# Kernel tuning notes

Hardware: AMD Instinct MI355X
Metric: run time of the kernel (lower is better)

Reference implementation:

```python
import jax, jax.numpy as jnp
import numpy as np

N = 50000      # nodes
E = 800000     # edges
IN = 32        # raw node feature dim
PE = 15        # laplacian PE dim (k)
HID = 128      # hidden
HEADS = 4
C = HID // HEADS
G = 64         # graphs in batch
L = 4          # num layers (shared weights!)


def setup_inputs() -> dict:
    key = jax.random.key(0)
    ks = jax.random.split(key, 24)
    s = 0.05
    p = lambda k, shape: jax.random.normal(k, shape, dtype=jnp.float32) * s
    inp = {
        "x": jax.random.normal(ks[0], (N, IN), dtype=jnp.float32),
        "edge_index": jax.random.randint(ks[1], (2, E), 0, N, dtype=jnp.int32),
        "batch": jnp.sort(jax.random.randint(ks[2], (N,), 0, G, dtype=jnp.int32)),
        "lap_pe": jax.random.normal(ks[3], (N, PE), dtype=jnp.float32),
        # node_in: Linear(IN+PE -> HID)
        "node_in_w": p(ks[4], (HID, IN + PE)), "node_in_b": p(ks[5], (HID,)),
        # shared TransformerConv params
        "Wq": p(ks[6], (HID, HID)), "bq": p(ks[7], (HID,)),
        "Wk": p(ks[8], (HID, HID)), "bk": p(ks[9], (HID,)),
        "Wv": p(ks[10], (HID, HID)), "bv": p(ks[11], (HID,)),
        "Wskip": p(ks[12], (HID, HID)), "bskip": p(ks[13], (HID,)),
        "Wbeta": p(ks[14], (1, 3 * HID)),  # bias=False in PyG
        # attentional aggregation gate: Linear(HID,HID)->ReLU->Linear(HID,1)
        "g1_w": p(ks[15], (HID, HID)), "g1_b": p(ks[16], (HID,)),
        "g2_w": p(ks[17], (1, HID)), "g2_b": p(ks[18], (1,)),
        # readout: Linear(HID,HID)->ReLU->Linear(HID,1)
        "r1_w": p(ks[19], (HID, HID)), "r1_b": p(ks[20], (HID,)),
        "r2_w": p(ks[21], (1, HID)), "r2_b": p(ks[22], (1,)),
    }
    return inp


def _transformer_conv(x, src, dst, Wq, bq, Wk, bk, Wv, bv, Wskip, bskip, Wbeta):
    # projections -> [N, HEADS, C]
    q = (x @ Wq.T + bq).reshape(N, HEADS, C)
    k = (x @ Wk.T + bk).reshape(N, HEADS, C)
    v = (x @ Wv.T + bv).reshape(N, HEADS, C)
    # edge attention logits: [E, HEADS]
    alpha = jnp.einsum('ehc,ehc->eh', q[dst], k[src]) / jnp.sqrt(jnp.float32(C))
    # segment softmax over destination node
    amax = jax.ops.segment_max(alpha, dst, num_segments=N)        # [N, HEADS]
    ex = jnp.exp(alpha - amax[dst])
    denom = jax.ops.segment_sum(ex, dst, num_segments=N)          # [N, HEADS]
    attn = ex / denom[dst]                                        # [E, HEADS]
    # weighted scatter-add of values
    msg = v[src] * attn[:, :, None]                               # [E, HEADS, C]
    out = jax.ops.segment_sum(msg, dst, num_segments=N).reshape(N, HID)
    # beta-gated skip connection (beta=True, root_weight=True)
    x_r = x @ Wskip.T + bskip
    beta = jax.nn.sigmoid(jnp.concatenate([out, x_r, out - x_r], axis=-1) @ Wbeta.T)
    return beta * x_r + (1.0 - beta) * out


def reference(x, edge_index, batch, lap_pe, node_in_w, node_in_b,
              Wq, bq, Wk, bk, Wv, bv, Wskip, bskip, Wbeta,
              g1_w, g1_b, g2_w, g2_b, r1_w, r1_b, r2_w, r2_b):
    src, dst = edge_index[0], edge_index[1]
    h = jnp.concatenate([x, lap_pe], axis=-1) @ node_in_w.T + node_in_b  # [N, HID]
    for _ in range(L):  # same conv instance reused -> shared weights
        h = jax.nn.relu(h + _transformer_conv(h, src, dst, Wq, bq, Wk, bk,
                                              Wv, bv, Wskip, bskip, Wbeta))
    # attentional aggregation over graphs
    gate = jax.nn.relu(h @ g1_w.T + g1_b) @ g2_w.T + g2_b                # [N, 1]
    gmax = jax.ops.segment_max(gate, batch, num_segments=G)
    gex = jnp.exp(gate - gmax[batch])
    gden = jax.ops.segment_sum(gex, batch, num_segments=G)
    w = gex / gden[batch]                                                # [N, 1]
    g = jax.ops.segment_sum(w * h, batch, num_segments=G)                # [G, HID]
    out = jax.nn.relu(g @ r1_w.T + r1_b) @ r2_w.T + r2_b                 # [G, 1]
    return out.squeeze(-1)
```

## Files before the change

kernel.cpp:

```cpp
#include <hip/hip_runtime.h>

#define NN 50000
#define EE 800000
#define INF 32
#define PEF 15
#define HID 128
#define GG 64
#define NLAYERS 4
#define NBLK 196
#define NBUCK 49
#define ECH 4096
#define EBLK 196

typedef __bf16 bf16;
typedef __attribute__((ext_vector_type(8))) bf16 bf16x8;
typedef __attribute__((ext_vector_type(4))) float f32x4;
typedef __attribute__((ext_vector_type(2))) float f32x2;

__device__ __forceinline__ float wave_allsum(float v) {
  #pragma unroll
  for (int off = 1; off < 64; off <<= 1) v += __shfl_xor(v, off);
  return v;
}

__device__ __forceinline__ float bflo(unsigned u) {
  return __builtin_bit_cast(float, u << 16);
}
__device__ __forceinline__ float bfhi(unsigned u) {
  return __builtin_bit_cast(float, u & 0xffff0000u);
}
__device__ __forceinline__ unsigned short f2bf(float v) {
  unsigned b = __builtin_bit_cast(unsigned, v);
  unsigned r = (b + 0x7fffu + ((b >> 16) & 1u)) >> 16;
  return (unsigned short)r;
}
__device__ __forceinline__ unsigned bfpack(float lo, float hi) {
  return (unsigned)f2bf(lo) | ((unsigned)f2bf(hi) << 16);
}
__device__ __forceinline__ unsigned fp8pack4(float a, float b, float c, float d) {
  unsigned lo = (unsigned)__builtin_amdgcn_cvt_pk_fp8_f32(a, b, 0, false) & 0xffffu;
  unsigned hi = (unsigned)__builtin_amdgcn_cvt_pk_fp8_f32(c, d, 0, false) & 0xffffu;
  return lo | (hi << 16);
}

__global__ void pack_weights_kernel(const float* __restrict__ Wq, const float* __restrict__ Wk,
                                    const float* __restrict__ Wv, const float* __restrict__ Ws,
                                    const float* __restrict__ bq, const float* __restrict__ bk,
                                    const float* __restrict__ bv, const float* __restrict__ bs,
                                    unsigned short* __restrict__ Wcatb, float* __restrict__ bcat) {
  int idx = blockIdx.x * blockDim.x + threadIdx.x;
  if (idx >= 512 * 128) return;
  int o = idx >> 7, j = idx & 127;
  int w = o >> 7, r = o & 127;
  const float* W = (w == 0) ? Wq : (w == 1) ? Wk : (w == 2) ? Wv : Ws;
  Wcatb[idx] = f2bf(W[r * 128 + j]);
  if (j == 0) {
    const float* b = (w == 0) ? bq : (w == 1) ? bk : (w == 2) ? bv : bs;
    bcat[o] = b[r];
  }
}

__global__ void pack_nwtb_kernel(const float* __restrict__ niw, unsigned short* __restrict__ nwtb) {
  int idx = blockIdx.x * blockDim.x + threadIdx.x;
  if (idx >= 128 * 64) return;
  int n = idx >> 6, j = idx & 63;
  nwtb[idx] = (j < INF + PEF) ? f2bf(niw[n * (INF + PEF) + j]) : (unsigned short)0;
}

__global__ void pack_g1_kernel(const float* __restrict__ g1w, unsigned short* __restrict__ g1wb) {
  int idx = blockIdx.x * blockDim.x + threadIdx.x;
  if (idx >= 128 * 128) return;
  g1wb[idx] = f2bf(g1w[idx]);
}

__global__ __launch_bounds__(256) void xpe_pack_kernel(const float* __restrict__ x,
    const float* __restrict__ pe, unsigned* __restrict__ xpeb4) {
  int n = blockIdx.x * 256 + threadIdx.x;
  if (n >= NN) return;
  unsigned ou[32];
  const float4* xr = (const float4*)(x + (size_t)n * INF);
  #pragma unroll
  for (int i = 0; i < 8; i++) {
    float4 v = xr[i];
    ou[2 * i] = bfpack(v.x, v.y);
    ou[2 * i + 1] = bfpack(v.z, v.w);
  }
  const float* pr = pe + (size_t)n * PEF;
  float p[16];
  #pragma unroll
  for (int i = 0; i < PEF; i++) p[i] = pr[i];
  p[15] = 0.f;
  #pragma unroll
  for (int i = 0; i < 8; i++) ou[16 + i] = bfpack(p[2 * i], p[2 * i + 1]);
  #pragma unroll
  for (int i = 24; i < 32; i++) ou[i] = 0u;
  unsigned* dst = xpeb4 + (size_t)n * 32;
  #pragma unroll
  for (int i = 0; i < 8; i++) ((uint4*)dst)[i] = *(uint4*)&ou[4 * i];
}

__global__ __launch_bounds__(256) void nodein_gemm_kernel(
    const bf16* __restrict__ A, const bf16* __restrict__ B,
    const float* __restrict__ bias, int M,
    float* __restrict__ h, unsigned* __restrict__ hbf4) {
  __shared__ float lds[128 * 64];
  const int t = threadIdx.x;
  const int w = t >> 6, lane = t & 63;
  const int m0 = blockIdx.x * 128;
  const int n0 = blockIdx.y * 64;
  const int lrow = lane & 15, lk = (lane >> 4) * 8;
  int ra = m0 + w * 32 + lrow;      if (ra > M - 1) ra = M - 1;
  int rb = m0 + w * 32 + 16 + lrow; if (rb > M - 1) rb = M - 1;
  const bf16* a0p = A + (size_t)ra * 64 + lk;
  const bf16* a1p = A + (size_t)rb * 64 + lk;
  const bf16* bp  = B + (size_t)(n0 + lrow) * 64 + lk;
  f32x4 acc[2][4] = {};
  #pragma unroll
  for (int ks = 0; ks < 2; ks++) {
    bf16x8 a0 = *(const bf16x8*)(a0p + ks * 32);
    bf16x8 a1 = *(const bf16x8*)(a1p + ks * 32);
    #pragma unroll
    for (int nj = 0; nj < 4; nj++) {
      bf16x8 b = *(const bf16x8*)(bp + (size_t)nj * 1024 + ks * 32);
      acc[0][nj] = __builtin_amdgcn_mfma_f32_16x16x32_bf16(a0, b, acc[0][nj], 0, 0, 0);
      acc[1][nj] = __builtin_amdgcn_mfma_f32_16x16x32_bf16(a1, b, acc[1][nj], 0, 0, 0);
    }
  }
  const int rbase = (lane >> 4) * 4;
  #pragma unroll
  for (int mi = 0; mi < 2; mi++) {
    #pragma unroll
    for (int nj = 0; nj < 4; nj++) {
      #pragma unroll
      for (int r = 0; r < 4; r++) {
        int ml = w * 32 + mi * 16 + rbase + r;
        int col = nj * 16 + lrow;
        lds[ml * 64 + (col ^ ((ml & 7) << 2))] = acc[mi][nj][r] + bias[n0 + col];
      }
    }
  }
  __syncthreads();
  #pragma unroll
  for (int kk = 0; kk < 2; kk++) {
    int u = t + kk * 256;
    int r = u & 127, s = u >> 7;
    int m = m0 + r;
    if (m >= M) continue;
    float ff[16];
    #pragma unroll
    for (int j = 0; j < 4; j++) {
      int c = s * 16 + j * 4;
      *(float4*)(ff + j * 4) = *(const float4*)(lds + r * 64 + (c ^ ((r & 7) << 2)));
    }
    int c0 = n0 + s * 16;
    float4* hp = (float4*)(h + (size_t)m * 128 + c0);
    #pragma unroll
    for (int j = 0; j < 4; j++) hp[j] = *(float4*)(ff + j * 4);
    unsigned o[8];
    #pragma unroll
    for (int i = 0; i < 8; i++) o[i] = bfpack(ff[2 * i], ff[2 * i + 1]);
    uint4* hb = (uint4*)(hbf4 + (size_t)m * 64 + (c0 >> 1));
    hb[0] = *(uint4*)&o[0];
    hb[1] = *(uint4*)&o[4];
  }
}

__global__ void count_kernel(const int* __restrict__ dst, int* __restrict__ counts) {
  int e = blockIdx.x * blockDim.x + threadIdx.x;
  if (e >= EE) return;
  atomicAdd(&counts[dst[e]], 1);
}

__global__ __launch_bounds__(256) void bsum_kernel(const int* __restrict__ counts,
                                                   int* __restrict__ bsum) {
  int b = blockIdx.x, t = threadIdx.x;
  int i = b * 256 + t;
  int v = (i < NN) ? counts[i] : 0;
  #pragma unroll
  for (int off = 1; off < 64; off <<= 1) v += __shfl_xor(v, off);
  __shared__ int red[4];
  if ((t & 63) == 0) red[t >> 6] = v;
  __syncthreads();
  if (t == 0) bsum[b] = red[0] + red[1] + red[2] + red[3];
}

__global__ void bscan_kernel(const int* __restrict__ bsum, int* __restrict__ bbase) {
  int lane = threadIdx.x;
  int carry = 0;
  for (int c = 0; c < NBLK; c += 64) {
    int i = c + lane;
    int v = (i < NBLK) ? bsum[i] : 0;
    int x = v;
    #pragma unroll
    for (int off = 1; off < 64; off <<= 1) {
      int u = __shfl_up(x, off);
      if (lane >= off) x += u;
    }
    if (i < NBLK) bbase[i] = carry + x - v;
    carry += __shfl(x, 63);
  }
}

__global__ __launch_bounds__(256) void rowptr_kernel(const int* __restrict__ counts,
    const int* __restrict__ bbase, int* __restrict__ row_ptr) {
  int b = blockIdx.x, t = threadIdx.x;
  int lane = t & 63, wid = t >> 6;
  int i = b * 256 + t;
  int v = (i < NN) ? counts[i] : 0;
  int x = v;
  #pragma unroll
  for (int off = 1; off < 64; off <<= 1) {
    int u = __shfl_up(x, off);
    if (lane >= off) x += u;
  }
  __shared__ int wsum[4];
  if (lane == 63) wsum[wid] = x;
  __syncthreads();
  int offs = bbase[b];
  for (int k = 0; k < wid; k++) offs += wsum[k];
  int incl = offs + x;
  if (i < NN) row_ptr[i + 1] = incl;
  if (b == 0 && t == 0) row_ptr[0] = 0;
}

__global__ __launch_bounds__(256) void binhist_kernel(const int* __restrict__ dst,
                                                      int* __restrict__ blockHist) {
  __shared__ int hist[NBUCK];
  int t = threadIdx.x;
  if (t < NBUCK) hist[t] = 0;
  __syncthreads();
  int base = blockIdx.x * ECH;
  int end = base + ECH; if (end > EE) end = EE;
  for (int i = base + t; i < end; i += 256) atomicAdd(&hist[dst[i] >> 10], 1);
  __syncthreads();
  if (t < NBUCK) blockHist[blockIdx.x * NBUCK + t] = hist[t];
}

__global__ void bscan2_kernel(const int* __restrict__ blockHist,
    int* __restrict__ blockBase, int* __restrict__ bucket_base) {
  int t = threadIdx.x;
  int tot = 0;
  if (t < NBUCK)
    for (int b = 0; b < EBLK; b++) tot += blockHist[b * NBUCK + t];
  int x = tot;
  #pragma unroll
  for (int off = 1; off < 64; off <<= 1) {
    int u = __shfl_up(x, off);
    if (t >= off) x += u;
  }
  int excl = x - tot;
  if (t < NBUCK) bucket_base[t] = excl;
  if (t == NBUCK - 1) bucket_base[NBUCK] = excl + tot;
  if (t < NBUCK) {
    int run = excl;
    for (int b = 0; b < EBLK; b++) {
      blockBase[b * NBUCK + t] = run;
      run += blockHist[b * NBUCK + t];
    }
  }
}

__global__ __launch_bounds__(256) void binwrite_kernel(const int* __restrict__ src,
    const int* __restrict__ dst, const int* __restrict__ blockBase,
    unsigned* __restrict__ binned) {
  __shared__ int cur[NBUCK];
  int t = threadIdx.x;
  if (t < NBUCK) cur[t] = blockBase[blockIdx.x * NBUCK + t];
  __syncthreads();
  int base = blockIdx.x * ECH;
  int end = base + ECH; if (end > EE) end = EE;
  for (int i = base + t; i < end; i += 256) {
    int d = dst[i];
    int p = atomicAdd(&cur[d >> 10], 1);
    binned[p] = (unsigned)src[i] | ((unsigned)(d & 1023) << 16);
  }
}

__global__ __launch_bounds__(512) void scatter2_kernel(const unsigned* __restrict__ binned,
    const int* __restrict__ row_ptr, const int* __restrict__ bucket_base,
    unsigned short* __restrict__ srcs16) {
  __shared__ int cur[1024];
  int g = blockIdx.x, t = threadIdx.x;
  int nbase = g << 10;
  for (int j = t; j < 1024; j += 512) {
    int node = nbase + j;
    cur[j] = (node < NN) ? row_ptr[node] : 0;
  }
  __syncthreads();
  int s0 = bucket_base[g], s1 = bucket_base[g + 1];
  for (int i = s0 + t; i < s1; i += 512) {
    unsigned pr = binned[i];
    int p = atomicAdd(&cur[pr >> 16], 1);
    srcs16[p] = (unsigned short)(pr & 0xffffu);
  }
}

__global__ void gptr_kernel(const int* __restrict__ batch, int* __restrict__ gptr) {
  int g = threadIdx.x;
  if (g > GG) return;
  if (g == GG) { gptr[GG] = NN; return; }
  int lo = 0, hi = NN;
  while (lo < hi) {
    int mid = (lo + hi) >> 1;
    if (batch[mid] < g) lo = mid + 1; else hi = mid;
  }
  gptr[g] = lo;
}

__global__ __launch_bounds__(512) void gemm0_kernel(
    const bf16* __restrict__ A, const bf16* __restrict__ B,
    const float* __restrict__ bias, int M,
    unsigned short* __restrict__ qbb, unsigned char* __restrict__ kvb,
    unsigned short* __restrict__ xrbb) {
  __shared__ float lds[64 * 128];
  const int t = threadIdx.x;
  const int w = t >> 6, lane = t & 63;
  const int wm = w >> 2, wn = w & 3;
  const int mb = blockIdx.x * 64;
  const int m0 = mb + wm * 32;
  const int n0 = wn * 128;
  const int lrow = lane & 15, lk = (lane >> 4) * 8;
  int ra = m0 + lrow;      if (ra > M - 1) ra = M - 1;
  int rb = m0 + 16 + lrow; if (rb > M - 1) rb = M - 1;
  const bf16* a0p = A + (size_t)ra * 128 + lk;
  const bf16* a1p = A + (size_t)rb * 128 + lk;
  const bf16* bp  = B + (size_t)(n0 + lrow) * 128 + lk;
  f32x4 acc[2][8] = {};
  #pragma unroll
  for (int ks = 0; ks < 4; ks++) {
    bf16x8 a0 = *(const bf16x8*)(a0p + ks * 32);
    bf16x8 a1 = *(const bf16x8*)(a1p + ks * 32);
    #pragma unroll
    for (int nj = 0; nj < 8; nj++) {
      bf16x8 b = *(const bf16x8*)(bp + (size_t)nj * 2048 + ks * 32);
      acc[0][nj] = __builtin_amdgcn_mfma_f32_16x16x32_bf16(a0, b, acc[0][nj], 0, 0, 0);
      acc[1][nj] = __builtin_amdgcn_mfma_f32_16x16x32_bf16(a1, b, acc[1][nj], 0, 0, 0);
    }
  }
  const int rbase = (lane >> 4) * 4;
  const int rr = t & 63, ss = t >> 6;
  const int m = mb + rr;
  #pragma unroll
  for (int g = 0; g < 4; g++) {
    if (wn == g) {
      #pragma unroll
      for (int mi = 0; mi < 2; mi++) {
        #pragma unroll
        for (int nj = 0; nj < 8; nj++) {
          #pragma unroll
          for (int r = 0; r < 4; r++) {
            int row = wm * 32 + mi * 16 + rbase + r;
            int col = nj * 16 + lrow;
            lds[row * 128 + (col ^ ((row & 7) << 2))] = acc[mi][nj][r] + bias[g * 128 + col];
          }
        }
      }
    }
    __syncthreads();
    if (m < M) {
      float ff[16];
      #pragma unroll
      for (int j = 0; j < 4; j++) {
        int c = ss * 16 + j * 4;
        *(float4*)(ff + j * 4) = *(const float4*)(lds + rr * 128 + (c ^ ((rr & 7) << 2)));
      }
      int c0 = ss * 16;
      if (g == 0) {
        unsigned o[8];
        #pragma unroll
        for (int i = 0; i < 8; i++) o[i] = bfpack(ff[2 * i], ff[2 * i + 1]);
        uint4* dq = (uint4*)(qbb + (size_t)m * 128 + c0);
        dq[0] = *(uint4*)&o[0];
        dq[1] = *(uint4*)&o[4];
      } else if (g == 1 || g == 2) {
        unsigned o[4];
        #pragma unroll
        for (int i = 0; i < 4; i++)
          o[i] = fp8pack4(ff[4 * i], ff[4 * i + 1], ff[4 * i + 2], ff[4 * i + 3]);
        int cell = c0 >> 3;
        int voff = (g == 1) ? 0 : 8;
        unsigned char* bp8 = kvb + (size_t)m * 256;
        uint2 w0; w0.x = o[0]; w0.y = o[1];
        uint2 w1; w1.x = o[2]; w1.y = o[3];
        *(uint2*)(bp8 + cell * 16 + voff) = w0;
        *(uint2*)(bp8 + (cell + 1) * 16 + voff) = w1;
      } else {
        unsigned o[8];
        #pragma unroll
        for (int i = 0; i < 8; i++) o[i] = bfpack(ff[2 * i], ff[2 * i + 1]);
        uint4* dx = (uint4*)(xrbb + (size_t)m * 128 + c0);
        dx[0] = *(uint4*)&o[0];
        dx[1] = *(uint4*)&o[4];
      }
    }
    __syncthreads();
  }
}

__global__ __launch_bounds__(512) void gemm1_gate_kernel(
    const bf16* __restrict__ A, const bf16* __restrict__ B,
    const float* __restrict__ b1, const float* __restrict__ g2w,
    const float* __restrict__ g2b, int M, float* __restrict__ gx) {
  const int w = threadIdx.x >> 6, lane = threadIdx.x & 63;
  const int m0 = blockIdx.x * 128 + w * 16;
  const int lrow = lane & 15, lk = (lane >> 4) * 8;
  int ra = m0 + lrow; if (ra > M - 1) ra = M - 1;
  const bf16* ap = A + (size_t)ra * 128 + lk;
  const bf16* bp = B + (size_t)lrow * 128 + lk;
  f32x4 acc[8] = {};
  #pragma unroll
  for (int ks = 0; ks < 4; ks++) {
    bf16x8 a = *(const bf16x8*)(ap + ks * 32);
    #pragma unroll
    for (int nj = 0; nj < 8; nj++) {
      bf16x8 b = *(const bf16x8*)(bp + (size_t)nj * 2048 + ks * 32);
      acc[nj] = __builtin_amdgcn_mfma_f32_16x16x32_bf16(a, b, acc[nj], 0, 0, 0);
    }
  }
  float g2v[8], b1v[8];
  #pragma unroll
  for (int nj = 0; nj < 8; nj++) {
    g2v[nj] = g2w[nj * 16 + lrow];
    b1v[nj] = b1[nj * 16 + lrow];
  }
  const float b2 = g2b[0];
  const int rbase = (lane >> 4) * 4;
  #pragma unroll
  for (int r = 0; r < 4; r++) {
    int m = m0 + rbase + r;
    float d = 0.f;
    #pragma unroll
    for (int nj = 0; nj < 8; nj++)
      d += fmaxf(acc[nj][r] + b1v[nj], 0.f) * g2v[nj];
    d += __shfl_xor(d, 1);
    d += __shfl_xor(d, 2);
    d += __shfl_xor(d, 4);
    d += __shfl_xor(d, 8);
    if (lrow == 0 && m < M) gx[m] = __expf(d + b2);
  }
}

__global__ __launch_bounds__(256) void attn_beta_kernel(
    const unsigned short* __restrict__ qbb,
    const unsigned char* __restrict__ kvb,
    const int* __restrict__ row_ptr, const unsigned short* __restrict__ srcs,
    const unsigned* __restrict__ xrb4,
    const float* __restrict__ Wbeta,
    float* __restrict__ h, unsigned* __restrict__ hbf4) {
  __shared__ float xlds[4][128];
  const int wid = threadIdx.x >> 6;
  const int wv = blockIdx.x * 4 + wid;
  const int lane = threadIdx.x & 63;
  const int sl = lane & 15;
  const int eg = lane >> 4;
  float qf[8];
  {
    bf16x8 qv = *(const bf16x8*)((const bf16*)qbb + (size_t)wv * 128 + sl * 8);
    #pragma unroll
    for (int j = 0; j < 8; j++) qf[j] = (float)qv[j];
  }
  const int e0 = row_ptr[wv], e1 = row_ptr[wv + 1];
  const float C = 0.25503486f;
  float dex = 0.f;
  float acc[8] = {0, 0, 0, 0, 0, 0, 0, 0};

#define PROC(cell, valid)                                                   \
  {                                                                         \
    f32x2 k0 = __builtin_amdgcn_cvt_pk_f32_fp8((cell).x, false);            \
    f32x2 k1 = __builtin_amdgcn_cvt_pk_f32_fp8((cell).x, true);             \
    f32x2 k2 = __builtin_amdgcn_cvt_pk_f32_fp8((cell).y, false);            \
    f32x2 k3 = __builtin_amdgcn_cvt_pk_f32_fp8((cell).y, true);             \
    float p = qf[0] * k0.x + qf[1] * k0.y + qf[2] * k1.x + qf[3] * k1.y     \
            + qf[4] * k2.x + qf[5] * k2.y + qf[6] * k3.x + qf[7] * k3.y;    \
    p += __shfl_xor(p, 1);                                                  \
    p += __shfl_xor(p, 2);                                                  \
    float ex = (valid) ? exp2f(p * C) : 0.f;                                \
    dex += ex;                                                              \
    f32x2 v0 = __builtin_amdgcn_cvt_pk_f32_fp8((cell).z, false);            \
    f32x2 v1 = __builtin_amdgcn_cvt_pk_f32_fp8((cell).z, true);             \
    f32x2 v2 = __builtin_amdgcn_cvt_pk_f32_fp8((cell).w, false);            \
    f32x2 v3 = __builtin_amdgcn_cvt_pk_f32_fp8((cell).w, true);             \
    acc[0] += ex * v0.x; acc[1] += ex * v0.y;                               \
    acc[2] += ex * v1.x; acc[3] += ex * v1.y;                               \
    acc[4] += ex * v2.x; acc[5] += ex * v2.y;                               \
    acc[6] += ex * v3.x; acc[7] += ex * v3.y;                               \
  }

  for (int base = e0; base < e1; base += 64) {
    int rem = e1 - base;
    int cnt = rem < 64 ? rem : 64;
    int mysrc = (lane < rem) ? (int)srcs[base + lane] : 0;
    int i = 0;
    for (; i + 4 < cnt; i += 8) {
      int sea = __shfl(mysrc, i + eg);
      int seb = __shfl(mysrc, i + 4 + eg);
      uint4 ca = *(const uint4*)(kvb + (size_t)sea * 256 + sl * 16);
      uint4 cb = *(const uint4*)(kvb + (size_t)seb * 256 + sl * 16);
      PROC(ca, true);
      PROC(cb, (i + 4 + eg < cnt));
    }
    if (i < cnt) {
      int sea = __shfl(mysrc, i + eg);
      uint4 ca = *(const uint4*)(kvb + (size_t)sea * 256 + sl * 16);
      PROC(ca, (i + eg < cnt));
    }
  }
#undef PROC

  dex += __shfl_xor(dex, 16);
  dex += __shfl_xor(dex, 32);
  #pragma unroll
  for (int j = 0; j < 8; j++) {
    acc[j] += __shfl_xor(acc[j], 16);
    acc[j] += __shfl_xor(acc[j], 32);
  }
  float inv = (e1 > e0) ? 1.f / dex : 0.f;
  if (eg == 0) {
    #pragma unroll
    for (int j = 0; j < 8; j++) xlds[wid][sl * 8 + j] = acc[j] * inv;
  }
  __syncthreads();
  float ox = xlds[wid][2 * lane];
  float oy = xlds[wid][2 * lane + 1];
  unsigned xu = xrb4[(size_t)wv * 64 + lane];
  float xx = bflo(xu), xy = bfhi(xu);
  const float2* wb = (const float2*)Wbeta;
  float2 wo = wb[lane], wx = wb[64 + lane], wd = wb[128 + lane];
  float part = ox * wo.x + oy * wo.y + xx * wx.x + xy * wx.y
             + (ox - xx) * wd.x + (oy - xy) * wd.y;
  part = wave_allsum(part);
  float beta = 1.f / (1.f + __expf(-part));
  float2* hp = (float2*)(h + (size_t)wv * 128);
  float2 h2 = hp[lane];
  float r0 = fmaxf(h2.x + beta * xx + (1.f - beta) * ox, 0.f);
  float r1 = fmaxf(h2.y + beta * xy + (1.f - beta) * oy, 0.f);
  h2.x = r0; h2.y = r1;
  hp[lane] = h2;
  hbf4[(size_t)wv * 64 + lane] = bfpack(r0, r1);
}

__global__ __launch_bounds__(256) void gden_kernel(const float* __restrict__ gx,
    const int* __restrict__ gptr, float* __restrict__ gden) {
  int g = blockIdx.x, t = threadIdx.x;
  int n0 = gptr[g], n1 = gptr[g + 1];
  float s = 0.f;
  for (int n = n0 + t; n < n1; n += 256) s += gx[n];
  s = wave_allsum(s);
  __shared__ float red[4];
  if ((t & 63) == 0) red[t >> 6] = s;
  __syncthreads();
  if (t == 0) gden[g] = red[0] + red[1] + red[2] + red[3];
}

__global__ __launch_bounds__(128) void gagg_kernel(const float* __restrict__ gx,
    const float* __restrict__ h, const int* __restrict__ gptr,
    float* __restrict__ gfeat_raw) {
  int g = blockIdx.x;
  int c = blockIdx.y;
  int d = threadIdx.x;
  int n0 = gptr[g], n1 = gptr[g + 1];
  float acc = 0.f;
  for (int n = n0 + c; n < n1; n += 32) acc += gx[n] * h[(size_t)n * 128 + d];
  atomicAdd(&gfeat_raw[g * 128 + d], acc);
}

__global__ __launch_bounds__(128) void readout_kernel(const float* __restrict__ gfeat_raw,
    const float* __restrict__ gden,
    const float* __restrict__ r1w, const float* __restrict__ r1b,
    const float* __restrict__ r2w, const float* __restrict__ r2b,
    float* __restrict__ out) {
  int g = blockIdx.x;
  int u = threadIdx.x;
  __shared__ float sh[128];
  __shared__ float red[128];
  float dv = gden[g];
  float inv = (dv > 0.f) ? 1.f / dv : 0.f;
  sh[u] = gfeat_raw[g * 128 + u] * inv;
  __syncthreads();
  float tacc = r1b[u];
  for (int j = 0; j < 128; j++) tacc += sh[j] * r1w[u * 128 + j];
  tacc = fmaxf(tacc, 0.f);
  red[u] = tacc * r2w[u];
  __syncthreads();
  for (int off = 64; off > 0; off >>= 1) {
    if (u < off) red[u] += red[u + off];
    __syncthreads();
  }
  if (u == 0) out[g] = red[0] + r2b[0];
}

extern "C" void kernel_launch(void* const* d_in, const int* in_sizes, int n_in,
                              void* d_out, int out_size, void* d_ws, size_t ws_size,
                              hipStream_t stream) {
  (void)in_sizes; (void)n_in; (void)out_size; (void)ws_size;
  const float* x     = (const float*)d_in[0];
  const int*   ei    = (const int*)d_in[1];
  const int*   batch = (const int*)d_in[2];
  const float* pe    = (const float*)d_in[3];
  const float* niw   = (const float*)d_in[4];
  const float* nib   = (const float*)d_in[5];
  const float* Wq    = (const float*)d_in[6];
  const float* bq    = (const float*)d_in[7];
  const float* Wk    = (const float*)d_in[8];
  const float* bk    = (const float*)d_in[9];
  const float* Wv    = (const float*)d_in[10];
  const float* bv    = (const float*)d_in[11];
  const float* Wsk   = (const float*)d_in[12];
  const float* bsk   = (const float*)d_in[13];
  const float* Wbeta = (const float*)d_in[14];
  const float* g1w   = (const float*)d_in[15];
  const float* g1b   = (const float*)d_in[16];
  const float* g2w   = (const float*)d_in[17];
  const float* g2b   = (const float*)d_in[18];
  const float* r1w   = (const float*)d_in[19];
  const float* r1b   = (const float*)d_in[20];
  const float* r2w   = (const float*)d_in[21];
  const float* r2b   = (const float*)d_in[22];
  float* out = (float*)d_out;

  float* ws = (float*)d_ws;
  float* h     = ws; ws += (size_t)NN * 128;
  float* qbbf  = ws; ws += (size_t)NN * 64;
  float* kvbf  = ws; ws += (size_t)NN * 64;
  float* xrbf  = ws; ws += (size_t)NN * 64;
  float* hbff  = ws; ws += (size_t)NN * 64;
  float* xpebf = ws; ws += (size_t)NN * 32;
  float* Wcatf = ws; ws += 512 * 64;
  float* g1wbf = ws; ws += 128 * 64;
  float* nwtbf = ws; ws += 128 * 32;
  float* bcat  = ws; ws += 512;
  float* gx    = ws; ws += NN;
  float* gfeat = ws; ws += GG * 128;
  float* gden  = ws; ws += GG;
  int* row_ptr = (int*)ws;
  int* counts   = row_ptr + (NN + 1);
  int* bsum     = counts + NN;
  int* bbase    = bsum + NBLK;
  int* gptr     = bbase + NBLK;
  int* blockHist= gptr + (GG + 1);
  int* blockBase= blockHist + EBLK * NBUCK;
  int* bucketB  = blockBase + EBLK * NBUCK;
  unsigned* binned = (unsigned*)(bucketB + (NBUCK + 1));
  unsigned short* srcs16 = (unsigned short*)(binned + EE);

  unsigned short* qbb   = (unsigned short*)qbbf;
  unsigned char*  kvb   = (unsigned char*)kvbf;
  unsigned short* xrbb  = (unsigned short*)xrbf;
  unsigned short* hbf   = (unsigned short*)hbff;
  unsigned short* Wcatb = (unsigned short*)Wcatf;
  unsigned short* g1wb  = (unsigned short*)g1wbf;
  unsigned short* nwtb  = (unsigned short*)nwtbf;
  const int* src = ei;
  const int* dst = ei + EE;

  hipMemsetAsync(counts, 0, NN * sizeof(int), stream);
  hipMemsetAsync(gfeat, 0, GG * 128 * sizeof(float), stream);
  pack_weights_kernel<<<(512 * 128 + 255) / 256, 256, 0, stream>>>(
      Wq, Wk, Wv, Wsk, bq, bk, bv, bsk, Wcatb, bcat);
  pack_nwtb_kernel<<<(128 * 64 + 255) / 256, 256, 0, stream>>>(niw, nwtb);
  pack_g1_kernel<<<(128 * 128 + 255) / 256, 256, 0, stream>>>(g1w, g1wb);
  xpe_pack_kernel<<<NBLK, 256, 0, stream>>>(x, pe, (unsigned*)xpebf);
  count_kernel<<<(EE + 255) / 256, 256, 0, stream>>>(dst, counts);
  bsum_kernel<<<NBLK, 256, 0, stream>>>(counts, bsum);
  bscan_kernel<<<1, 64, 0, stream>>>(bsum, bbase);
  rowptr_kernel<<<NBLK, 256, 0, stream>>>(counts, bbase, row_ptr);
  binhist_kernel<<<EBLK, 256, 0, stream>>>(dst, blockHist);
  bscan2_kernel<<<1, 64, 0, stream>>>(blockHist, blockBase, bucketB);
  binwrite_kernel<<<EBLK, 256, 0, stream>>>(src, dst, blockBase, binned);
  scatter2_kernel<<<NBUCK, 512, 0, stream>>>(binned, row_ptr, bucketB, srcs16);
  gptr_kernel<<<1, 128, 0, stream>>>(batch, gptr);

  const int MB0 = (NN + 127) / 128;
  const int MB64 = (NN + 63) / 64;
  nodein_gemm_kernel<<<dim3(MB0, 2), 256, 0, stream>>>(
      (const bf16*)xpebf, (const bf16*)nwtb, nib, NN, h, (unsigned*)hbf);

  for (int l = 0; l < NLAYERS; l++) {
    gemm0_kernel<<<MB64, 512, 0, stream>>>(
        (const bf16*)hbf, (const bf16*)Wcatb, bcat, NN, qbb, kvb, xrbb);
    attn_beta_kernel<<<12500, 256, 0, stream>>>(
        qbb, kvb, row_ptr, srcs16, (const unsigned*)xrbb, Wbeta, h, (unsigned*)hbf);
  }

  gemm1_gate_kernel<<<MB0, 512, 0, stream>>>(
      (const bf16*)hbf, (const bf16*)g1wb, g1b, g2w, g2b, NN, gx);
  gden_kernel<<<GG, 256, 0, stream>>>(gx, gptr, gden);
  gagg_kernel<<<dim3(GG, 32), 128, 0, stream>>>(gx, h, gptr, gfeat);
  readout_kernel<<<GG, 128, 0, stream>>>(gfeat, gden, r1w, r1b, r2w, r2b, out);
}
```

Before: 623.6 us.

## Retile QKV/skip projection GEMM into 128x64 tiles over a 2D grid

The fused projection GEMM changes from 64-row blocks that compute all 512 output columns in four serialized LDS-staged epilogue rounds to a 2D grid of 128x64 tiles. Each block now runs one epilogue pass and one barrier, and picks the q/k/v/skip output format from blockIdx.y. This removes the per-group barrier serialization and raises the block count for better occupancy. In exchange, each A row is re-read across 8 column blocks instead of once.

```diff
diff --git a/kernel.cpp b/kernel.cpp
--- a/kernel.cpp
+++ b/kernel.cpp
@@ -307,78 +307,76 @@
   gptr[g] = lo;
 }
 
-__global__ __launch_bounds__(512) void gemm0_kernel(
+__global__ __launch_bounds__(256) void gemm0_kernel(
     const bf16* __restrict__ A, const bf16* __restrict__ B,
     const float* __restrict__ bias, int M,
     unsigned short* __restrict__ qbb, unsigned char* __restrict__ kvb,
     unsigned short* __restrict__ xrbb) {
-  __shared__ float lds[64 * 128];
+  __shared__ float lds[128 * 64];
   const int t = threadIdx.x;
   const int w = t >> 6, lane = t & 63;
-  const int wm = w >> 2, wn = w & 3;
-  const int mb = blockIdx.x * 64;
-  const int m0 = mb + wm * 32;
-  const int n0 = wn * 128;
+  const int m0 = blockIdx.x * 128;
+  const int by = blockIdx.y;
+  const int n0 = by * 64;
   const int lrow = lane & 15, lk = (lane >> 4) * 8;
-  int ra = m0 + lrow;      if (ra > M - 1) ra = M - 1;
-  int rb = m0 + 16 + lrow; if (rb > M - 1) rb = M - 1;
+  int ra = m0 + w * 32 + lrow;      if (ra > M - 1) ra = M - 1;
+  int rb = m0 + w * 32 + 16 + lrow; if (rb > M - 1) rb = M - 1;
   const bf16* a0p = A + (size_t)ra * 128 + lk;
   const bf16* a1p = A + (size_t)rb * 128 + lk;
   const bf16* bp  = B + (size_t)(n0 + lrow) * 128 + lk;
-  f32x4 acc[2][8] = {};
+  f32x4 acc[2][4] = {};
   #pragma unroll
   for (int ks = 0; ks < 4; ks++) {
     bf16x8 a0 = *(const bf16x8*)(a0p + ks * 32);
     bf16x8 a1 = *(const bf16x8*)(a1p + ks * 32);
     #pragma unroll
-    for (int nj = 0; nj < 8; nj++) {
+    for (int nj = 0; nj < 4; nj++) {
       bf16x8 b = *(const bf16x8*)(bp + (size_t)nj * 2048 + ks * 32);
       acc[0][nj] = __builtin_amdgcn_mfma_f32_16x16x32_bf16(a0, b, acc[0][nj], 0, 0, 0);
       acc[1][nj] = __builtin_amdgcn_mfma_f32_16x16x32_bf16(a1, b, acc[1][nj], 0, 0, 0);
     }
   }
   const int rbase = (lane >> 4) * 4;
-  const int rr = t & 63, ss = t >> 6;
-  const int m = mb + rr;
-  #pragma unroll
-  for (int g = 0; g < 4; g++) {
-    if (wn == g) {
+  #pragma unroll
+  for (int mi = 0; mi < 2; mi++) {
+    #pragma unroll
+    for (int nj = 0; nj < 4; nj++) {
       #pragma unroll
-      for (int mi = 0; mi < 2; mi++) {
-        #pragma unroll
-        for (int nj = 0; nj < 8; nj++) {
-          #pragma unroll
-          for (int r = 0; r < 4; r++) {
-            int row = wm * 32 + mi * 16 + rbase + r;
-            int col = nj * 16 + lrow;
-            lds[row * 128 + (col ^ ((row & 7) << 2))] = acc[mi][nj][r] + bias[g * 128 + col];
-          }
-        }
+      for (int r = 0; r < 4; r++) {
+        int ml = w * 32 + mi * 16 + rbase + r;
+        int col = nj * 16 + lrow;
+        lds[ml * 64 + (col ^ ((ml & 7) << 2))] = acc[mi][nj][r] + bias[n0 + col];
       }
     }
-    __syncthreads();
+  }
+  __syncthreads();
+  #pragma unroll
+  for (int kk = 0; kk < 2; kk++) {
+    int u = t + kk * 256;
+    int r = u & 127, s = u >> 7;
+    int m = m0 + r;
+    float ff[16];
+    #pragma unroll
+    for (int j = 0; j < 4; j++) {
+      int c = s * 16 + j * 4;
+      *(float4*)(ff + j * 4) = *(const float4*)(lds + r * 64 + (c ^ ((r & 7) << 2)));
+    }
     if (m < M) {
-      float ff[16];
-      #pragma unroll
-      for (int j = 0; j < 4; j++) {
-        int c = ss * 16 + j * 4;
-        *(float4*)(ff + j * 4) = *(const float4*)(lds + rr * 128 + (c ^ ((rr & 7) << 2)));
-      }
-      int c0 = ss * 16;
-      if (g == 0) {
+      int c0 = (by & 1) * 64 + s * 16;
+      if (by < 2) {
         unsigned o[8];
         #pragma unroll
         for (int i = 0; i < 8; i++) o[i] = bfpack(ff[2 * i], ff[2 * i + 1]);
         uint4* dq = (uint4*)(qbb + (size_t)m * 128 + c0);
         dq[0] = *(uint4*)&o[0];
         dq[1] = *(uint4*)&o[4];
-      } else if (g == 1 || g == 2) {
+      } else if (by < 6) {
         unsigned o[4];
         #pragma unroll
         for (int i = 0; i < 4; i++)
           o[i] = fp8pack4(ff[4 * i], ff[4 * i + 1], ff[4 * i + 2], ff[4 * i + 3]);
         int cell = c0 >> 3;
-        int voff = (g == 1) ? 0 : 8;
+        int voff = (by < 4) ? 0 : 8;
         unsigned char* bp8 = kvb + (size_t)m * 256;
         uint2 w0; w0.x = o[0]; w0.y = o[1];
         uint2 w1; w1.x = o[2]; w1.y = o[3];
@@ -393,7 +391,6 @@
         dx[1] = *(uint4*)&o[4];
       }
     }
-    __syncthreads();
   }
 }
 
@@ -671,12 +668,11 @@
   gptr_kernel<<<1, 128, 0, stream>>>(batch, gptr);
 
   const int MB0 = (NN + 127) / 128;
-  const int MB64 = (NN + 63) / 64;
   nodein_gemm_kernel<<<dim3(MB0, 2), 256, 0, stream>>>(
       (const bf16*)xpebf, (const bf16*)nwtb, nib, NN, h, (unsigned*)hbf);
 
   for (int l = 0; l < NLAYERS; l++) {
-    gemm0_kernel<<<MB64, 512, 0, stream>>>(
+    gemm0_kernel<<<dim3(MB0, 8), 256, 0, stream>>>(
         (const bf16*)hbf, (const bf16*)Wcatb, bcat, NN, qbb, kvb, xrbb);
     attn_beta_kernel<<<12500, 256, 0, stream>>>(
         qbb, kvb, row_ptr, srcs16, (const unsigned*)xrbb, Wbeta, h, (unsigned*)hbf);
```

New measurement: 548.9 us. 1.14x faster.
